# Kernel tuning notes

Measured on AMD Instinct MI355X. Metric: run time of the kernel, lower is better.

Reference implementation:

```python
import jax, jax.numpy as jnp
import numpy as np

N, E = 50000, 800000
NFEAT, NHID = 128, 128


def setup_inputs() -> dict:
    key = jax.random.key(0)
    ks = jax.random.split(key, 10)
    s = 1.0 / np.sqrt(NFEAT)
    inp = {
        "x": jax.random.normal(ks[0], (N, NFEAT), dtype=jnp.float32),
        "edge_index": jax.random.randint(ks[1], (2, E), 0, N, dtype=jnp.int32),
        "head": 0,
        # Relation params (nn.Linear weights, [out, in], bias=False)
        "gamma1_w": jax.random.uniform(ks[2], (NFEAT, NFEAT), jnp.float32, -s, s),
        "gamma2_w": jax.random.uniform(ks[3], (NFEAT, NFEAT), jnp.float32, -s, s),
        "beta1_w": jax.random.uniform(ks[4], (NFEAT, NFEAT), jnp.float32, -s, s),
        "beta2_w": jax.random.uniform(ks[5], (NFEAT, NFEAT), jnp.float32, -s, s),
        "r": jax.random.uniform(ks[6], (1, NFEAT), jnp.float32, -s, s),
        # GCNConv params: lin (bias=False) + conv bias
        "lin_w": jax.random.uniform(ks[7], (NHID, NFEAT), jnp.float32, -s, s),
        "bias": jnp.zeros((NHID,), dtype=jnp.float32),
    }
    return inp


def _lrelu(v):
    return jnp.where(v >= 0, v, 0.2 * v)  # LeakyReLU(0.2)


def _forward(x, edge_index, gamma1_w, gamma2_w, beta1_w, beta2_w, r, lin_w, bias):
    n = x.shape[0]
    row, col = edge_index[0], edge_index[1]
    ones_e = jnp.ones((edge_index.shape[1],), dtype=x.dtype)

    # num_neighbor = scatter_add(ones, row); neighbor = scatter_mean(x[col], row)
    num_neighbor = jax.ops.segment_sum(ones_e, row, num_segments=n)  # [N]
    neigh_sum = jax.ops.segment_sum(x[col], row, num_segments=n)      # [N, F]
    neighbor = neigh_sum / jnp.maximum(num_neighbor, 1.0)[:, None]

    # Relation (ablation=0): FiLM-style translation vector
    gamma = _lrelu(x @ gamma1_w.T + neighbor @ gamma2_w.T) + 1.0
    beta = _lrelu(x @ beta1_w.T + neighbor @ beta2_w.T)
    output = x + (gamma * r + beta) - neighbor                        # [N, F]

    xw = x @ lin_w.T                                                  # [N, H]
    loop = jnp.arange(n, dtype=row.dtype)
    row2 = jnp.concatenate([row, loop])
    col2 = jnp.concatenate([col, loop])
    deg = jax.ops.segment_sum(jnp.ones_like(row2, dtype=x.dtype), col2, num_segments=n)
    dinv = jnp.where(deg > 0, jax.lax.rsqrt(deg), 0.0)
    norm = dinv[row2] * dinv[col2]                                    # [E+N]
    h_k = jax.ops.segment_sum(norm[:, None] * xw[row2], col2, num_segments=n) + bias

    # tail branch (head=False, ablation=0): h_s = output, projected by gc.lin.weight
    h_s = output @ lin_w.T
    h_k = (h_k + h_s) / (num_neighbor + 1.0)[:, None]
    return h_k, output


def reference(x, edge_index, head, gamma1_w, gamma2_w, beta1_w, beta2_w, r, lin_w, bias):
    # head is a static Python int (0 -> tail branch, the full fused path)
    assert not head
    return _forward(x, edge_index, gamma1_w, gamma2_w, beta1_w, beta2_w, r, lin_w, bias)
```

## Files before the change

### kernel.cpp

```cpp
#include <hip/hip_runtime.h>

#define NN 50000
#define NE 800000
#define NF 128
#define QS (NN * 32)

#define SHIFT 8
#define NB 196
#define PBLOCKS 128
#define PCHUNK ((NE + PBLOCKS - 1) / PBLOCKS)

#define NTILES ((NN + 63) / 64)
#define FBLOCKS 512

#define CVX_BLOCKS 3125
#define CVW_BLOCKS 320
#define PREP_BLOCKS (CVX_BLOCKS + CVW_BLOCKS + PBLOCKS)

typedef __attribute__((ext_vector_type(4))) float f32x4;
typedef __attribute__((ext_vector_type(8))) short bf16x8;

__device__ __forceinline__ short f2bf(float f) {
    unsigned u = __float_as_uint(f);
    u += 0x7FFF + ((u >> 16) & 1);
    return (short)(u >> 16);
}
__device__ __forceinline__ float bf2f(short s) {
    return __uint_as_float(((unsigned)(unsigned short)s) << 16);
}

__global__ __launch_bounds__(256) void prep_kernel(
    const float* __restrict__ x, const float* __restrict__ g1,
    const float* __restrict__ g2, const float* __restrict__ b1,
    const float* __restrict__ b2, const float* __restrict__ lin,
    const int* __restrict__ ei, short* __restrict__ xq,
    short* __restrict__ wbf, int* __restrict__ gcnt) {
    __shared__ int cnt[2 * NB];
    int bid = blockIdx.x;
    int t = threadIdx.x;

    if (bid < CVX_BLOCKS) {
        int i = bid * 256 + t;
        if (i < NN * 16) {
            int n = i >> 4, c = i & 15;
            int q = c >> 2, sub = c & 3;
            float4 a = ((const float4*)x)[i * 2];
            float4 b = ((const float4*)x)[i * 2 + 1];
            bf16x8 v;
            v[0] = f2bf(a.x); v[1] = f2bf(a.y); v[2] = f2bf(a.z); v[3] = f2bf(a.w);
            v[4] = f2bf(b.x); v[5] = f2bf(b.y); v[6] = f2bf(b.z); v[7] = f2bf(b.w);
            *(bf16x8*)(xq + (size_t)q * QS + n * 32 + sub * 8) = v;
        }
        return;
    }
    if (bid < CVX_BLOCKS + CVW_BLOCKS) {
        int i = (bid - CVX_BLOCKS) * 256 + t;
        if (i < 5 * NF * NF) {
            int m = i >> 14, off = i & (NF * NF - 1);
            float v = (m == 0) ? g1[off] : (m == 1) ? g2[off] : (m == 2) ? b1[off]
                    : (m == 3) ? b2[off] : lin[off];
            wbf[i] = f2bf(v);
        }
        return;
    }
    int pb = bid - CVX_BLOCKS - CVW_BLOCKS;
    for (int i = t; i < 2 * NB; i += 256) cnt[i] = 0;
    __syncthreads();
    int lo = pb * PCHUNK;
    int hi = min(lo + PCHUNK, NE);
    for (int j = lo + t; j < hi; j += 256) {
        int r = ei[j];
        int c = ei[NE + j];
        atomicAdd(&cnt[r >> SHIFT], 1);
        atomicAdd(&cnt[NB + (c >> SHIFT)], 1);
    }
    __syncthreads();
    for (int i = t; i < 2 * NB; i += 256)
        if (cnt[i]) atomicAdd(&gcnt[i], cnt[i]);
}

__global__ __launch_bounds__(256) void p1_scan_kernel(const int* __restrict__ gcnt,
                                                      int* __restrict__ baseR,
                                                      int* __restrict__ baseC,
                                                      int* __restrict__ gcur) {
    __shared__ int s[256];
    int t = threadIdx.x;
    int v = (t < NB) ? gcnt[t] : 0;
    s[t] = v;
    __syncthreads();
    for (int off = 1; off < 256; off <<= 1) {
        int u = (t >= off) ? s[t - off] : 0;
        __syncthreads();
        s[t] += u;
        __syncthreads();
    }
    if (t < NB) {
        int excl = s[t] - v;
        baseR[t] = excl;
        gcur[t] = excl;
        if (t == NB - 1) baseR[NB] = s[t];
    }
    __syncthreads();
    int v2 = (t < NB) ? gcnt[NB + t] : 0;
    s[t] = v2;
    __syncthreads();
    for (int off = 1; off < 256; off <<= 1) {
        int u = (t >= off) ? s[t - off] : 0;
        __syncthreads();
        s[t] += u;
        __syncthreads();
    }
    if (t < NB) {
        int excl = s[t] - v2;
        baseC[t] = excl;
        gcur[NB + t] = excl;
        if (t == NB - 1) baseC[NB] = s[t];
    }
}

__global__ __launch_bounds__(256) void p2_partition_kernel(const int* __restrict__ ei,
                                                           int* __restrict__ gcur,
                                                           unsigned* __restrict__ partR,
                                                           unsigned* __restrict__ partC) {
    __shared__ int cnt[2 * NB];
    __shared__ int res[2 * NB];
    int t = threadIdx.x;
    for (int i = t; i < 2 * NB; i += 256) cnt[i] = 0;
    __syncthreads();
    int lo = blockIdx.x * PCHUNK;
    int hi = min(lo + PCHUNK, NE);
    for (int j = lo + t; j < hi; j += 256) {
        int r = ei[j];
        int c = ei[NE + j];
        atomicAdd(&cnt[r >> SHIFT], 1);
        atomicAdd(&cnt[NB + (c >> SHIFT)], 1);
    }
    __syncthreads();
    for (int i = t; i < 2 * NB; i += 256) {
        int n = cnt[i];
        res[i] = n ? atomicAdd(&gcur[i], n) : 0;
        cnt[i] = 0;
    }
    __syncthreads();
    for (int j = lo + t; j < hi; j += 256) {
        int r = ei[j];
        int c = ei[NE + j];
        int bR = r >> SHIFT;
        int sR = atomicAdd(&cnt[bR], 1);
        partR[res[bR] + sR] = ((unsigned)(r & 255) << 17) | (unsigned)c;
        int bC = NB + (c >> SHIFT);
        int sC = atomicAdd(&cnt[bC], 1);
        partC[res[bC] + sC] = ((unsigned)(c & 255) << 17) | (unsigned)r;
    }
}

__global__ __launch_bounds__(256) void p3_build_kernel(
    const unsigned* __restrict__ partR, const unsigned* __restrict__ partC,
    const int* __restrict__ baseR, const int* __restrict__ baseC,
    int* __restrict__ offs_r, int* __restrict__ offs_c,
    int* __restrict__ csr_r, int* __restrict__ csr_c,
    int* __restrict__ degr, float* __restrict__ dinv,
    const short* __restrict__ xq, short* __restrict__ xdq) {
    int side = blockIdx.x / NB;
    int b = blockIdx.x - side * NB;
    const unsigned* part = side ? partC : partR;
    const int* base = side ? baseC : baseR;
    int* offs = side ? offs_c : offs_r;
    int* csr = side ? csr_c : csr_r;

    __shared__ int deg[256];
    __shared__ int cur[256];
    __shared__ float dinvs[256];
    int t = threadIdx.x;
    int s0 = base[b], s1 = base[b + 1];
    deg[t] = 0;
    __syncthreads();
    for (int j = s0 + t; j < s1; j += 256)
        atomicAdd(&deg[part[j] >> 17], 1);
    __syncthreads();
    int myDeg = deg[t];
    for (int off = 1; off < 256; off <<= 1) {
        int u = (t >= off) ? deg[t - off] : 0;
        __syncthreads();
        deg[t] += u;
        __syncthreads();
    }
    int excl = deg[t] - myDeg;
    int node = (b << SHIFT) + t;
    if (node <= NN) offs[node] = s0 + excl;
    if (node < NN) {
        if (side == 0) degr[node] = myDeg;
        else {
            float dc = rsqrtf((float)myDeg + 1.0f);
            dinv[node] = dc;
            dinvs[t] = dc;
        }
    }
    cur[t] = excl;
    __syncthreads();
    for (int j = s0 + t; j < s1; j += 256) {
        unsigned en = part[j];
        int k = en >> 17;
        int p = atomicAdd(&cur[k], 1);
        csr[s0 + p] = (int)(en & 0x1FFFFu);
    }
    if (side == 1) {
        #pragma unroll 1
        for (int pass = 0; pass < 4; ++pass) {
            int nl = pass * 64 + (t >> 2);
            int ci = t & 3;
            int node2 = (b << SHIFT) + nl;
            if (node2 < NN) {
                float dc = dinvs[nl];
                #pragma unroll
                for (int qi = 0; qi < 4; ++qi) {
                    bf16x8 v = *(const bf16x8*)(xq + (size_t)qi * QS + node2 * 32 + ci * 8);
                    bf16x8 o;
                    #pragma unroll
                    for (int k = 0; k < 8; ++k) o[k] = f2bf(dc * bf2f(v[k]));
                    *(bf16x8*)(xdq + (size_t)qi * QS + node2 * 32 + ci * 8) = o;
                }
            }
        }
    }
}

__global__ __launch_bounds__(256) void gather_fused_kernel(
    const int* __restrict__ offs_r, const int* __restrict__ csr_r,
    const int* __restrict__ offs_c, const int* __restrict__ csr_c,
    const short* __restrict__ xq, const short* __restrict__ xdq,
    const float* __restrict__ dinv,
    short* __restrict__ nbq, short* __restrict__ zq) {
    int lane8 = blockIdx.x & 7;
    int side = lane8 >> 2;
    int q = lane8 & 3;
    int grp = blockIdx.x >> 3;
    int t = threadIdx.x;
    int g = grp * 16 + (t >> 4);
    int slot = (t >> 2) & 3;
    int fl = t & 3;

    const short* xb = (side ? xdq : xq) + (size_t)q * QS + fl * 8;
    const int* offs = side ? offs_c : offs_r;
    const int* csr  = side ? csr_c  : csr_r;

    int s = offs[g], e = offs[g + 1];
    int deg = e - s;

    float acc[8] = {0.f, 0.f, 0.f, 0.f, 0.f, 0.f, 0.f, 0.f};

    if (s & 1) {
        if (slot == 0) {
            bf16x8 v = *(const bf16x8*)(xb + csr[s] * 32);
            #pragma unroll
            for (int k = 0; k < 8; ++k) acc[k] += bf2f(v[k]);
        }
        ++s;
    }
    int npairs = (e - s) >> 1;
    int p = slot;
    for (; p + 4 < npairs; p += 8) {
        int2 c0 = *(const int2*)(csr + s + 2 * p);
        int2 c1 = *(const int2*)(csr + s + 2 * p + 8);
        bf16x8 v0 = *(const bf16x8*)(xb + c0.x * 32);
        bf16x8 v1 = *(const bf16x8*)(xb + c0.y * 32);
        bf16x8 v2 = *(const bf16x8*)(xb + c1.x * 32);
        bf16x8 v3 = *(const bf16x8*)(xb + c1.y * 32);
        #pragma unroll
        for (int k = 0; k < 8; ++k)
            acc[k] += (bf2f(v0[k]) + bf2f(v1[k])) + (bf2f(v2[k]) + bf2f(v3[k]));
    }
    for (; p < npairs; p += 4) {
        int2 c0 = *(const int2*)(csr + s + 2 * p);
        bf16x8 v0 = *(const bf16x8*)(xb + c0.x * 32);
        bf16x8 v1 = *(const bf16x8*)(xb + c0.y * 32);
        #pragma unroll
        for (int k = 0; k < 8; ++k) acc[k] += bf2f(v0[k]) + bf2f(v1[k]);
    }
    if (((e - s) & 1) && slot == 0) {
        bf16x8 v = *(const bf16x8*)(xb + csr[e - 1] * 32);
        #pragma unroll
        for (int k = 0; k < 8; ++k) acc[k] += bf2f(v[k]);
    }

    #pragma unroll
    for (int k = 0; k < 8; ++k) {
        acc[k] += __shfl_xor(acc[k], 4);
        acc[k] += __shfl_xor(acc[k], 8);
    }

    if (slot == 0) {
        if (side == 0) {
            float invn = 1.0f / fmaxf((float)deg, 1.0f);
            bf16x8 o;
            #pragma unroll
            for (int k = 0; k < 8; ++k) o[k] = f2bf(acc[k] * invn);
            *(bf16x8*)(nbq + (size_t)q * QS + g * 32 + fl * 8) = o;
        } else {
            float dc = dinv[g];
            bf16x8 self = *(const bf16x8*)(xb + g * 32);
            bf16x8 zo;
            #pragma unroll
            for (int k = 0; k < 8; ++k) zo[k] = f2bf(dc * (acc[k] + bf2f(self[k])));
            *(bf16x8*)(zq + (size_t)q * QS + g * 32 + fl * 8) = zo;
        }
    }
}

__global__ __launch_bounds__(256, 2) void film_mfma_kernel(
    const short* __restrict__ xq, const short* __restrict__ nbq,
    const short* __restrict__ zq, const short* __restrict__ wbf,
    const float* __restrict__ rvec, const float* __restrict__ bias,
    const int* __restrict__ degr, float* __restrict__ outp,
    float* __restrict__ hko) {
    __shared__ short xs[64 * NF];
    __shared__ short ns[64 * NF];
    __shared__ short zs[64 * NF];

    int tid = threadIdx.x;
    int w = tid >> 6;
    int l = tid & 63;
    int lr = l & 15;
    int lg = l >> 4;

    bf16x8 wf[2][5][4];
    float rc[2], bc[2];
    #pragma unroll
    for (int j = 0; j < 2; ++j) {
        int col = (2 * w + j) * 16 + lr;
        #pragma unroll
        for (int m = 0; m < 5; ++m) {
            const short* wm = wbf + m * 16384 + col * NF;
            #pragma unroll
            for (int kb = 0; kb < 4; ++kb)
                wf[j][m][kb] = *(const bf16x8*)(wm + kb * 32 + lg * 8);
        }
        rc[j] = rvec[col];
        bc[j] = bias[col];
    }

    #pragma unroll 1
    for (int tile = blockIdx.x; tile < NTILES; tile += FBLOCKS) {
        int node0 = tile * 64;

        #pragma unroll
        for (int it = 0; it < 4; ++it) {
            int chunk = it * 256 + tid;
            int row = chunk >> 4;
            int c = chunk & 15;
            int grow = min(node0 + row, NN - 1);
            int swz = ((c ^ (row & 7)) << 3);
            size_t qoff = (size_t)(c >> 2) * QS + grow * 32 + (c & 3) * 8;
            *(bf16x8*)(xs + row * NF + swz) = *(const bf16x8*)(xq + qoff);
            *(bf16x8*)(ns + row * NF + swz) = *(const bf16x8*)(nbq + qoff);
            *(bf16x8*)(zs + row * NF + swz) = *(const bf16x8*)(zq + qoff);
        }
        __syncthreads();

        #pragma unroll 1
        for (int rg = 0; rg < 4; ++rg) {
            bf16x8 xf[4], nf[4];
            #pragma unroll
            for (int kb = 0; kb < 4; ++kb) {
                int row = rg * 16 + lr;
                int swz = (((kb * 4 + lg) ^ (row & 7)) << 3);
                xf[kb] = *(const bf16x8*)(xs + row * NF + swz);
                nf[kb] = *(const bf16x8*)(ns + row * NF + swz);
            }
            #pragma unroll
            for (int j = 0; j < 2; ++j) {
                f32x4 ag = {0.f, 0.f, 0.f, 0.f};
                f32x4 ab = {0.f, 0.f, 0.f, 0.f};
                #pragma unroll
                for (int kb = 0; kb < 4; ++kb) {
                    ag = __builtin_amdgcn_mfma_f32_16x16x32_bf16(xf[kb], wf[j][0][kb], ag, 0, 0, 0);
                    ag = __builtin_amdgcn_mfma_f32_16x16x32_bf16(nf[kb], wf[j][1][kb], ag, 0, 0, 0);
                    ab = __builtin_amdgcn_mfma_f32_16x16x32_bf16(xf[kb], wf[j][2][kb], ab, 0, 0, 0);
                    ab = __builtin_amdgcn_mfma_f32_16x16x32_bf16(nf[kb], wf[j][3][kb], ab, 0, 0, 0);
                }
                int col = (2 * w + j) * 16 + lr;
                #pragma unroll
                for (int q = 0; q < 4; ++q) {
                    int nl = rg * 16 + lg * 4 + q;
                    int ng = node0 + nl;
                    int addr = nl * NF + (((col >> 3) ^ (nl & 7)) << 3) + (col & 7);
                    float xv = bf2f(xs[addr]);
                    float nv = bf2f(ns[addr]);
                    float gp = ag[q], bp = ab[q];
                    float gamma = (gp >= 0.f ? gp : 0.2f * gp) + 1.0f;
                    float beta  = (bp >= 0.f ? bp : 0.2f * bp);
                    float o = xv + gamma * rc[j] + beta - nv;
                    if (ng < NN) outp[ng * NF + col] = o;
                    zs[addr] = f2bf(o + bf2f(zs[addr]));
                }
            }
        }
        __syncthreads();

        #pragma unroll 1
        for (int rg = 0; rg < 4; ++rg) {
            bf16x8 of[4];
            #pragma unroll
            for (int kb = 0; kb < 4; ++kb) {
                int row = rg * 16 + lr;
                int swz = (((kb * 4 + lg) ^ (row & 7)) << 3);
                of[kb] = *(const bf16x8*)(zs + row * NF + swz);
            }
            float invdq[4];
            #pragma unroll
            for (int q = 0; q < 4; ++q)
                invdq[q] = 1.0f / ((float)degr[min(node0 + rg * 16 + lg * 4 + q, NN - 1)] + 1.0f);
            #pragma unroll
            for (int j = 0; j < 2; ++j) {
                f32x4 as = {0.f, 0.f, 0.f, 0.f};
                #pragma unroll
                for (int kb = 0; kb < 4; ++kb)
                    as = __builtin_amdgcn_mfma_f32_16x16x32_bf16(of[kb], wf[j][4][kb], as, 0, 0, 0);
                int col = (2 * w + j) * 16 + lr;
                #pragma unroll
                for (int q = 0; q < 4; ++q) {
                    int ng = node0 + rg * 16 + lg * 4 + q;
                    if (ng < NN) hko[ng * NF + col] = (as[q] + bc[j]) * invdq[q];
                }
            }
        }
        __syncthreads();
    }
}

extern "C" void kernel_launch(void* const* d_in, const int* in_sizes, int n_in,
                              void* d_out, int out_size, void* d_ws, size_t ws_size,
                              hipStream_t stream) {
    const float* x    = (const float*)d_in[0];
    const int*   ei   = (const int*)d_in[1];
    const float* g1   = (const float*)d_in[3];
    const float* g2   = (const float*)d_in[4];
    const float* b1   = (const float*)d_in[5];
    const float* b2   = (const float*)d_in[6];
    const float* rv   = (const float*)d_in[7];
    const float* lin  = (const float*)d_in[8];
    const float* bias = (const float*)d_in[9];

    float* dinv = (float*)d_ws;
    int* degr   = (int*)(dinv + NN);
    int* offs_r = degr + NN;
    int* offs_c = offs_r + (NN + 2);
    int* csr_r  = offs_c + (NN + 2);
    int* csr_c  = csr_r + NE;
    unsigned* partR = (unsigned*)(csr_c + NE);
    unsigned* partC = partR + NE;
    int* gcnt   = (int*)(partC + NE);
    int* gcur   = gcnt + 2 * NB;
    int* baseR  = gcur + 2 * NB;
    int* baseC  = baseR + (NB + 1);
    uintptr_t p = (uintptr_t)(baseC + NB + 1);
    p = (p + 15) & ~(uintptr_t)15;
    short* xq   = (short*)p;
    short* nbq  = xq + 4 * QS;
    short* zq   = nbq + 4 * QS;
    short* xdq  = zq + 4 * QS;
    short* wbf  = xdq + 4 * QS;

    float* hko  = (float*)d_out;
    float* outp = hko + NN * NF;

    hipMemsetAsync(gcnt, 0, 2 * NB * sizeof(int), stream);

    prep_kernel<<<PREP_BLOCKS, 256, 0, stream>>>(x, g1, g2, b1, b2, lin, ei,
                                                 xq, wbf, gcnt);
    p1_scan_kernel<<<1, 256, 0, stream>>>(gcnt, baseR, baseC, gcur);
    p2_partition_kernel<<<PBLOCKS, 256, 0, stream>>>(ei, gcur, partR, partC);
    p3_build_kernel<<<2 * NB, 256, 0, stream>>>(partR, partC, baseR, baseC,
                                                offs_r, offs_c, csr_r, csr_c,
                                                degr, dinv, xq, xdq);
    gather_fused_kernel<<<((NN + 15) / 16) * 8, 256, 0, stream>>>(
        offs_r, csr_r, offs_c, csr_c, xq, xdq, dinv, nbq, zq);
    film_mfma_kernel<<<FBLOCKS, 256, 0, stream>>>(xq, nbq, zq, wbf, rv, bias, degr,
                                                  outp, hko);
}
```

Baseline: 162.5 us.

## Use packed f32x2 bf16 unpacking in gather and one tile per FiLM block

The gather kernel now accumulates bf16 neighbor rows as packed float2 pairs, unpacking each 32-bit word with a shift and a mask so the adds can map to packed FP32 instructions. The FiLM MFMA kernel drops its grid-stride tile loop and launches one block per 64-node tile, removing the trailing barrier. In exchange, every block reloads its per-wave weight fragments from global memory, so weight traffic goes up in return for more parallelism and no loop overhead.

```diff
diff --git a/kernel.cpp b/kernel.cpp
--- a/kernel.cpp
+++ b/kernel.cpp
@@ -11,13 +11,14 @@
 #define PCHUNK ((NE + PBLOCKS - 1) / PBLOCKS)
 
 #define NTILES ((NN + 63) / 64)
-#define FBLOCKS 512
+#define FBLOCKS NTILES
 
 #define CVX_BLOCKS 3125
 #define CVW_BLOCKS 320
 #define PREP_BLOCKS (CVX_BLOCKS + CVW_BLOCKS + PBLOCKS)
 
 typedef __attribute__((ext_vector_type(4))) float f32x4;
+typedef __attribute__((ext_vector_type(2))) float f32x2;
 typedef __attribute__((ext_vector_type(8))) short bf16x8;
 
 __device__ __forceinline__ short f2bf(float f) {
@@ -27,6 +28,18 @@
 }
 __device__ __forceinline__ float bf2f(short s) {
     return __uint_as_float(((unsigned)(unsigned short)s) << 16);
+}
+
+__device__ __forceinline__ void acc8(int4 v, f32x2* a) {
+    unsigned u;
+    u = (unsigned)v.x;
+    a[0] += (f32x2){__uint_as_float(u << 16), __uint_as_float(u & 0xffff0000u)};
+    u = (unsigned)v.y;
+    a[1] += (f32x2){__uint_as_float(u << 16), __uint_as_float(u & 0xffff0000u)};
+    u = (unsigned)v.z;
+    a[2] += (f32x2){__uint_as_float(u << 16), __uint_as_float(u & 0xffff0000u)};
+    u = (unsigned)v.w;
+    a[3] += (f32x2){__uint_as_float(u << 16), __uint_as_float(u & 0xffff0000u)};
 }
 
 __global__ __launch_bounds__(256) void prep_kernel(
@@ -247,14 +260,10 @@
     int s = offs[g], e = offs[g + 1];
     int deg = e - s;
 
-    float acc[8] = {0.f, 0.f, 0.f, 0.f, 0.f, 0.f, 0.f, 0.f};
+    f32x2 a[4] = {{0.f, 0.f}, {0.f, 0.f}, {0.f, 0.f}, {0.f, 0.f}};
 
     if (s & 1) {
-        if (slot == 0) {
-            bf16x8 v = *(const bf16x8*)(xb + csr[s] * 32);
-            #pragma unroll
-            for (int k = 0; k < 8; ++k) acc[k] += bf2f(v[k]);
-        }
+        if (slot == 0) acc8(*(const int4*)(xb + csr[s] * 32), a);
         ++s;
     }
     int npairs = (e - s) >> 1;
@@ -262,31 +271,27 @@
     for (; p + 4 < npairs; p += 8) {
         int2 c0 = *(const int2*)(csr + s + 2 * p);
         int2 c1 = *(const int2*)(csr + s + 2 * p + 8);
-        bf16x8 v0 = *(const bf16x8*)(xb + c0.x * 32);
-        bf16x8 v1 = *(const bf16x8*)(xb + c0.y * 32);
-        bf16x8 v2 = *(const bf16x8*)(xb + c1.x * 32);
-        bf16x8 v3 = *(const bf16x8*)(xb + c1.y * 32);
-        #pragma unroll
-        for (int k = 0; k < 8; ++k)
-            acc[k] += (bf2f(v0[k]) + bf2f(v1[k])) + (bf2f(v2[k]) + bf2f(v3[k]));
+        int4 v0 = *(const int4*)(xb + c0.x * 32);
+        int4 v1 = *(const int4*)(xb + c0.y * 32);
+        int4 v2 = *(const int4*)(xb + c1.x * 32);
+        int4 v3 = *(const int4*)(xb + c1.y * 32);
+        acc8(v0, a); acc8(v1, a); acc8(v2, a); acc8(v3, a);
     }
     for (; p < npairs; p += 4) {
         int2 c0 = *(const int2*)(csr + s + 2 * p);
-        bf16x8 v0 = *(const bf16x8*)(xb + c0.x * 32);
-        bf16x8 v1 = *(const bf16x8*)(xb + c0.y * 32);
-        #pragma unroll
-        for (int k = 0; k < 8; ++k) acc[k] += bf2f(v0[k]) + bf2f(v1[k]);
-    }
-    if (((e - s) & 1) && slot == 0) {
-        bf16x8 v = *(const bf16x8*)(xb + csr[e - 1] * 32);
-        #pragma unroll
-        for (int k = 0; k < 8; ++k) acc[k] += bf2f(v[k]);
-    }
+        int4 v0 = *(const int4*)(xb + c0.x * 32);
+        int4 v1 = *(const int4*)(xb + c0.y * 32);
+        acc8(v0, a); acc8(v1, a);
+    }
+    if (((e - s) & 1) && slot == 0)
+        acc8(*(const int4*)(xb + csr[e - 1] * 32), a);
 
     #pragma unroll
-    for (int k = 0; k < 8; ++k) {
-        acc[k] += __shfl_xor(acc[k], 4);
-        acc[k] += __shfl_xor(acc[k], 8);
+    for (int i = 0; i < 4; ++i) {
+        a[i].x += __shfl_xor(a[i].x, 4);
+        a[i].y += __shfl_xor(a[i].y, 4);
+        a[i].x += __shfl_xor(a[i].x, 8);
+        a[i].y += __shfl_xor(a[i].y, 8);
     }
 
     if (slot == 0) {
@@ -294,14 +299,20 @@
             float invn = 1.0f / fmaxf((float)deg, 1.0f);
             bf16x8 o;
             #pragma unroll
-            for (int k = 0; k < 8; ++k) o[k] = f2bf(acc[k] * invn);
+            for (int i = 0; i < 4; ++i) {
+                o[2 * i]     = f2bf(a[i].x * invn);
+                o[2 * i + 1] = f2bf(a[i].y * invn);
+            }
             *(bf16x8*)(nbq + (size_t)q * QS + g * 32 + fl * 8) = o;
         } else {
             float dc = dinv[g];
             bf16x8 self = *(const bf16x8*)(xb + g * 32);
             bf16x8 zo;
             #pragma unroll
-            for (int k = 0; k < 8; ++k) zo[k] = f2bf(dc * (acc[k] + bf2f(self[k])));
+            for (int i = 0; i < 4; ++i) {
+                zo[2 * i]     = f2bf(dc * (a[i].x + bf2f(self[2 * i])));
+                zo[2 * i + 1] = f2bf(dc * (a[i].y + bf2f(self[2 * i + 1])));
+            }
             *(bf16x8*)(zq + (size_t)q * QS + g * 32 + fl * 8) = zo;
         }
     }
@@ -339,8 +350,8 @@
         bc[j] = bias[col];
     }
 
-    #pragma unroll 1
-    for (int tile = blockIdx.x; tile < NTILES; tile += FBLOCKS) {
+    int tile = blockIdx.x;
+    {
         int node0 = tile * 64;
 
         #pragma unroll
@@ -424,7 +435,6 @@
                 }
             }
         }
-        __syncthreads();
     }
 }
 
```

New measurement: 168.6 us. +3.8%, slower.
